# Kernel tuning notes

Measured on AMD Instinct MI355X. Metric: run time of the kernel, lower is better.

The kernel has to match this reference:

```python
import jax, jax.numpy as jnp
import numpy as np

EPS = 1e-8


def normalize_points(p):
    # p: [..., D+1]; normalize feature part to unit L2 norm, fix sign by last coord
    f = p[..., :-1]
    h = p[..., -1:]
    zero_mask = jnp.all(f == 0, axis=-1, keepdims=True)
    f = jnp.where(zero_mask, jnp.ones_like(f), f)
    norm = jnp.linalg.norm(f, axis=-1, keepdims=True)
    nf = f / jnp.clip(norm, EPS)
    n = jnp.concatenate([nf, h], axis=-1)
    sign = jnp.sign(n[..., -1:])
    sign = jnp.where(sign == 0, jnp.ones_like(sign), sign)
    return n * sign


def uhg_transform(x, weight):
    # x: [M, D_in+1], weight: [D_out, D_in]
    f = x[..., :-1]
    h = x[..., -1:]
    t = jnp.matmul(f, weight.T)  # [M, D_out]
    norm = jnp.linalg.norm(t, axis=-1, keepdims=True)
    t = t / jnp.clip(norm, EPS)
    return normalize_points(jnp.concatenate([t, h], axis=-1))


def setup_inputs() -> dict:
    key = jax.random.key(0)
    k1, k2, k3, k4 = jax.random.split(key, 4)
    N, E = 20000, 320000
    D_IN, D_OUT = 256, 256  # in_features-1, out_features
    x = jax.random.normal(k1, (N, D_IN + 1), dtype=jnp.float32)
    edge_index = jax.random.randint(k2, (2, E), 0, N, dtype=jnp.int32)
    # orthogonal-ish init approximated by row-normalized gaussian weights
    W_self = jax.random.normal(k3, (D_OUT, D_IN), dtype=jnp.float32)
    W_self = W_self / jnp.clip(jnp.linalg.norm(W_self, axis=1, keepdims=True), EPS)
    W_neigh = jax.random.normal(k4, (D_OUT, D_IN), dtype=jnp.float32)
    W_neigh = W_neigh / jnp.clip(jnp.linalg.norm(W_neigh, axis=1, keepdims=True), EPS)
    return {"x": x, "W_self": W_self, "W_neigh": W_neigh, "edge_index": edge_index}


def reference(x, W_self, W_neigh, edge_index):
    N = x.shape[0]
    D_OUT = W_self.shape[0]
    x = normalize_points(x)
    row, col = edge_index[0], edge_index[1]

    self_trans = uhg_transform(x, W_self)              # [N, D_OUT+1]
    neigh_trans = uhg_transform(x[col], W_neigh)       # [E, D_OUT+1]

    # mean aggregation: scatter-add full (features + homogeneous), count-divide features only
    out = jnp.zeros((N, D_OUT + 1), dtype=x.dtype).at[:, -1].set(1.0)
    out = out.at[row].add(neigh_trans)
    count = jnp.zeros((N, 1), dtype=x.dtype).at[row].add(1.0)
    count = jnp.clip(count, 1.0)
    out = jnp.concatenate([out[:, :-1] / count, out[:, -1:]], axis=-1)
    out = normalize_points(out)

    # uhg_weighted_average(p1, p2, 0.5): elementwise blend then renormalize
    t = jnp.clip(0.5 / (1.0 - 0.5 + EPS), EPS, 1e8)
    p1 = normalize_points(self_trans)
    p2 = normalize_points(out)
    avg = (p1 * t + p2) / jnp.clip(t + 1.0, EPS)
    combined = normalize_points(avg)
    return normalize_points(combined)
```

## Files before the change

kernel.cpp:

```cpp
#include <hip/hip_runtime.h>
#include <hip/hip_bf16.h>

#define EPSF 1e-8f
#define CAP 64

typedef __attribute__((ext_vector_type(4))) float floatx4;
typedef __attribute__((ext_vector_type(2))) float floatx2;
typedef __attribute__((ext_vector_type(2))) long longx2;

__device__ inline unsigned short f2bf(float v) {
    union { float f; unsigned int u; } un; un.f = v;
    unsigned int r = (un.u + 0x7fffu + ((un.u >> 16) & 1u)) >> 16;
    return (unsigned short)r;
}
__device__ inline float bf2f(unsigned short u) {
    union { unsigned int i; float f; } un; un.i = ((unsigned int)u) << 16;
    return un.f;
}

__device__ inline unsigned char f2fp8(float v) {
#if __has_builtin(__builtin_amdgcn_cvt_pk_fp8_f32)
    return (unsigned char)(__builtin_amdgcn_cvt_pk_fp8_f32(v, 0.f, 0u, false) & 0xff);
#else
    union { float f; unsigned u; } x; x.f = v;
    unsigned s = x.u >> 31; x.u &= 0x7fffffffu;
    if (x.f != x.f || x.f == 0.f) return (unsigned char)(s << 7);
    int e = (int)((x.u >> 23) & 0xff) - 127 + 7;
    unsigned m = x.u & 0x7fffffu;
    unsigned char r;
    if (e >= 1) {
        unsigned keep = m >> 20, rest = m & 0xfffffu;
        keep += (rest > 0x80000u) || (rest == 0x80000u && (keep & 1));
        if (keep == 8) { keep = 0; e += 1; }
        if (e > 15) { e = 15; keep = 6; }
        r = (unsigned char)((e << 3) | keep);
    } else {
        int q = (int)(x.f * 512.f + 0.5f);
        if (q > 7) r = 0x08; else r = (unsigned char)q;
    }
    return (unsigned char)(r | (s << 7));
#endif
}
__device__ inline unsigned pk_fp8x4(float v0, float v1, float v2, float v3) {
#if __has_builtin(__builtin_amdgcn_cvt_pk_fp8_f32)
    unsigned u = __builtin_amdgcn_cvt_pk_fp8_f32(v0, v1, 0u, false);
    u = __builtin_amdgcn_cvt_pk_fp8_f32(v2, v3, u, true);
    return u;
#else
    return (unsigned)f2fp8(v0) | ((unsigned)f2fp8(v1) << 8)
         | ((unsigned)f2fp8(v2) << 16) | ((unsigned)f2fp8(v3) << 24);
#endif
}
__device__ inline floatx2 fp8x2_to_f32(unsigned int u, bool word) {
#if __has_builtin(__builtin_amdgcn_cvt_pk_f32_fp8)
    return word ? __builtin_amdgcn_cvt_pk_f32_fp8(u, true)
                : __builtin_amdgcn_cvt_pk_f32_fp8(u, false);
#else
    floatx2 out;
    #pragma unroll
    for (int i = 0; i < 2; ++i) {
        unsigned char b = (u >> ((word ? 16 : 0) + 8 * i)) & 0xff;
        unsigned s = (b >> 7) & 1, e = (b >> 3) & 15, m = b & 7;
        float v;
        if (e) { union { unsigned u2; float f; } x; x.u2 = (s << 31) | ((e + 120u) << 23) | (m << 20); v = x.f; }
        else   { v = (s ? -1.f : 1.f) * (float)m * 0.001953125f; }
        out[i] = v;
    }
    return out;
#endif
}

__global__ __launch_bounds__(512) void k_front(
        const float* __restrict__ x, const float* __restrict__ Ws,
        const float* __restrict__ Wn,
        unsigned char* __restrict__ Wswz,
        float* __restrict__ xh, int N) {
    int b = blockIdx.x, t = threadIdx.x;
    if (b < 32) {
        int idx = b * 512 + t;
        int t0 = (idx & 3) * 4;
        int lane = (idx >> 2) & 63;
        int p = (idx >> 8) & 3;
        int g = (idx >> 10) & 3;
        int wq = (idx >> 12) & 3;
        int q = lane >> 4, l16 = lane & 15;
        int row = wq * 64 + g * 16 + l16;
        int s = 2 * p + (t0 >> 3);
        int k0 = 32 * s + 8 * q + (t0 & 7);
        float4 vs = *reinterpret_cast<const float4*>(Ws + row * 256 + k0);
        float4 vn = *reinterpret_cast<const float4*>(Wn + row * 256 + k0);
        reinterpret_cast<unsigned*>(Wswz)[idx] = pk_fp8x4(vs.x, vs.y, vs.z, vs.w);
        reinterpret_cast<unsigned*>(Wswz)[16384 + idx] = pk_fp8x4(vn.x, vn.y, vn.z, vn.w);
    } else {
        int i = (b - 32) * 512 + t;
        if (i < N) xh[i] = fabsf(x[(size_t)i * 257 + 256]);
    }
}

__global__ __launch_bounds__(512, 8) void k_mid(
        const float* __restrict__ x,
        const unsigned char* __restrict__ Wswz,
        const int* __restrict__ ei,
        int* __restrict__ cnt, int* __restrict__ scol,
        unsigned short* __restrict__ selfb, unsigned char* __restrict__ yb8,
        int N, int E, int EB) {
    __shared__ __align__(16) unsigned char As[32][256];
    __shared__ float pss[8][32];
    __shared__ float sgnS[32];
    int b = blockIdx.x, tid = threadIdx.x;
    int T = gridDim.x;

    int ebBefore = (int)(((long)b * EB) / T);
    bool isBucket = ((int)(((long)(b + 1) * EB) / T)) != ebBefore;
    if (isBucket) {
        int e = ebBefore * 512 + tid;
        if (e < E) {
            int r = ei[e], c = ei[E + e];
            int pos = atomicAdd(&cnt[r], 1);
            if (pos < CAP) scol[r * CAP + pos] = c;
        }
        return;
    }

    int wave = tid >> 6, lane = tid & 63;
    int quad = lane >> 4, l16 = lane & 15;
    int mat = wave >> 2, wq = wave & 3;
    int row0 = (b - ebBefore) * 32;

    if (tid < 32) {
        int gr = row0 + tid; if (gr >= N) gr = N - 1;
        float h = x[(size_t)gr * 257 + 256];
        sgnS[tid] = (h < 0.f) ? -1.f : 1.f;
    }
    __syncthreads();

    #pragma unroll
    for (int ps = 0; ps < 4; ++ps) {
        int c = ps * 512 + tid;
        int row = c >> 6, k0 = (c & 63) * 4;
        int gr = row0 + row; if (gr >= N) gr = N - 1;
        float4 v = *reinterpret_cast<const float4*>(x + (size_t)gr * 257 + k0);
        float sg = sgnS[row];
        int s = k0 >> 5, q = (k0 >> 3) & 3, j0 = k0 & 7;
        int dst = (q * 64 + (s >> 1) * 16 + (s & 1) * 8 + j0 + row * 16) & 255;
        *reinterpret_cast<unsigned*>(&As[row][dst]) =
            pk_fp8x4(v.x * sg, v.y * sg, v.z * sg, v.w * sg);
    }
    __syncthreads();

    const unsigned char* Wb = Wswz + ((size_t)mat << 16) + ((size_t)wq << 14);
    int rowA = l16, rowB = 16 + l16;

    floatx4 acc[2][4];
    #pragma unroll
    for (int rt = 0; rt < 2; ++rt)
        #pragma unroll
        for (int g = 0; g < 4; ++g) acc[rt][g] = floatx4{0.f, 0.f, 0.f, 0.f};

    #pragma unroll
    for (int p = 0; p < 4; ++p) {
        longx2 a0 = *reinterpret_cast<const longx2*>(
            &As[rowA][(quad * 64 + p * 16 + rowA * 16) & 255]);
        longx2 a1 = *reinterpret_cast<const longx2*>(
            &As[rowB][(quad * 64 + p * 16 + rowB * 16) & 255]);
        #pragma unroll
        for (int g = 0; g < 4; ++g) {
            longx2 w = *reinterpret_cast<const longx2*>(
                Wb + (((g * 4 + p) * 64 + lane) << 4));
            acc[0][g] = __builtin_amdgcn_mfma_f32_16x16x32_fp8_fp8(a0[0], w[0], acc[0][g], 0, 0, 0);
            acc[1][g] = __builtin_amdgcn_mfma_f32_16x16x32_fp8_fp8(a1[0], w[0], acc[1][g], 0, 0, 0);
            acc[0][g] = __builtin_amdgcn_mfma_f32_16x16x32_fp8_fp8(a0[1], w[1], acc[0][g], 0, 0, 0);
            acc[1][g] = __builtin_amdgcn_mfma_f32_16x16x32_fp8_fp8(a1[1], w[1], acc[1][g], 0, 0, 0);
        }
    }

    #pragma unroll
    for (int rt = 0; rt < 2; ++rt) {
        float s[4];
        #pragma unroll
        for (int reg = 0; reg < 4; ++reg) {
            float v = 0.f;
            #pragma unroll
            for (int g = 0; g < 4; ++g) v += acc[rt][g][reg] * acc[rt][g][reg];
            #pragma unroll
            for (int o = 8; o > 0; o >>= 1) v += __shfl_down(v, o, 64);
            s[reg] = v;
        }
        if (l16 == 0) {
            #pragma unroll
            for (int reg = 0; reg < 4; ++reg)
                pss[wave][rt * 16 + quad * 4 + reg] = s[reg];
        }
    }
    __syncthreads();

    int wb = mat * 4;
    #pragma unroll
    for (int rt = 0; rt < 2; ++rt)
        #pragma unroll
        for (int reg = 0; reg < 4; ++reg) {
            int r32 = rt * 16 + quad * 4 + reg;
            int gr = row0 + r32;
            if (gr >= N) continue;
            float ss = pss[wb][r32] + pss[wb + 1][r32]
                     + pss[wb + 2][r32] + pss[wb + 3][r32];
            bool zero = (ss == 0.f);
            float scale = zero ? 0.f : (1.f / fmaxf(sqrtf(ss), EPSF));
            #pragma unroll
            for (int g = 0; g < 4; ++g) {
                int col = wq * 64 + 16 * g + l16;
                float val = zero ? 0.0625f : acc[rt][g][reg] * scale;
                if (mat == 0) selfb[(size_t)gr * 256 + col] = f2bf(val);
                else          yb8[(size_t)gr * 256 + col] = f2fp8(val);
            }
        }
}

__global__ __launch_bounds__(256) void k_agg_combine(
        const int* __restrict__ cnt, const int* __restrict__ scol,
        const unsigned char* __restrict__ yb8,
        const float* __restrict__ xh,
        const unsigned short* __restrict__ selfb,
        float* __restrict__ out, int N) {
    int wid = (blockIdx.x * 256 + threadIdx.x) >> 6;
    if (wid >= N) return;
    int lane = threadIdx.x & 63;
    int deg = cnt[wid]; if (deg > CAP) deg = CAP;
    int beg = wid * CAP;
    float a0 = 0.f, a1 = 0.f, a2 = 0.f, a3 = 0.f;
    float b0 = 0.f, b1 = 0.f, b2 = 0.f, b3 = 0.f;
    int e = beg, end = beg + deg;
    for (; e + 3 < end; e += 4) {
        int c0 = scol[e], c1 = scol[e + 1], c2 = scol[e + 2], c3 = scol[e + 3];
        unsigned u0 = *reinterpret_cast<const unsigned*>(yb8 + (size_t)c0 * 256 + lane * 4);
        unsigned u1 = *reinterpret_cast<const unsigned*>(yb8 + (size_t)c1 * 256 + lane * 4);
        unsigned u2 = *reinterpret_cast<const unsigned*>(yb8 + (size_t)c2 * 256 + lane * 4);
        unsigned u3 = *reinterpret_cast<const unsigned*>(yb8 + (size_t)c3 * 256 + lane * 4);
        floatx2 p;
        p = fp8x2_to_f32(u0, false); a0 += p[0]; a1 += p[1];
        p = fp8x2_to_f32(u0, true);  a2 += p[0]; a3 += p[1];
        p = fp8x2_to_f32(u1, false); b0 += p[0]; b1 += p[1];
        p = fp8x2_to_f32(u1, true);  b2 += p[0]; b3 += p[1];
        p = fp8x2_to_f32(u2, false); a0 += p[0]; a1 += p[1];
        p = fp8x2_to_f32(u2, true);  a2 += p[0]; a3 += p[1];
        p = fp8x2_to_f32(u3, false); b0 += p[0]; b1 += p[1];
        p = fp8x2_to_f32(u3, true);  b2 += p[0]; b3 += p[1];
    }
    for (; e < end; ++e) {
        int c0 = scol[e];
        unsigned u0 = *reinterpret_cast<const unsigned*>(yb8 + (size_t)c0 * 256 + lane * 4);
        floatx2 p;
        p = fp8x2_to_f32(u0, false); a0 += p[0]; a1 += p[1];
        p = fp8x2_to_f32(u0, true);  a2 += p[0]; a3 += p[1];
    }
    a0 += b0; a1 += b1; a2 += b2; a3 += b3;

    float hs = 0.f;
    for (int j = lane; j < deg; j += 64) hs += xh[scol[beg + j]];
    #pragma unroll
    for (int o = 32; o > 0; o >>= 1) hs += __shfl_xor(hs, o, 64);

    float cn = (deg > 0) ? (float)deg : 1.f;
    float m0 = a0 / cn, m1 = a1 / cn, m2 = a2 / cn, m3 = a3 / cn;
    float ss = m0 * m0 + m1 * m1 + m2 * m2 + m3 * m3;
    #pragma unroll
    for (int o = 32; o > 0; o >>= 1) ss += __shfl_xor(ss, o, 64);
    bool z = (ss == 0.f);
    float inv = 1.f / fmaxf(z ? 16.f : sqrtf(ss), EPSF);
    float o0 = (z ? 1.f : m0) * inv, o1 = (z ? 1.f : m1) * inv;
    float o2 = (z ? 1.f : m2) * inv, o3 = (z ? 1.f : m3) * inv;

    ushort4 s4 = *reinterpret_cast<const ushort4*>(selfb + (size_t)wid * 256 + lane * 4);
    float v0 = 0.5f * (bf2f(s4.x) + o0), v1 = 0.5f * (bf2f(s4.y) + o1);
    float v2 = 0.5f * (bf2f(s4.z) + o2), v3 = 0.5f * (bf2f(s4.w) + o3);
    float ss2 = v0 * v0 + v1 * v1 + v2 * v2 + v3 * v3;
    #pragma unroll
    for (int o = 32; o > 0; o >>= 1) ss2 += __shfl_xor(ss2, o, 64);
    bool z2 = (ss2 == 0.f);
    float inv2 = 1.f / fmaxf(z2 ? 16.f : sqrtf(ss2), EPSF);

    float* op = out + (size_t)wid * 257 + lane * 4;
    op[0] = (z2 ? 1.f : v0) * inv2;
    op[1] = (z2 ? 1.f : v1) * inv2;
    op[2] = (z2 ? 1.f : v2) * inv2;
    op[3] = (z2 ? 1.f : v3) * inv2;
    if (lane == 0) out[(size_t)wid * 257 + 256] = 0.5f * (xh[wid] + 1.f + hs);
}

extern "C" void kernel_launch(void* const* d_in, const int* in_sizes, int n_in,
                              void* d_out, int out_size, void* d_ws, size_t ws_size,
                              hipStream_t stream) {
    const float* x  = (const float*)d_in[0];
    const float* Ws = (const float*)d_in[1];
    const float* Wn = (const float*)d_in[2];
    const int*   ei = (const int*)d_in[3];
    int N = in_sizes[0] / 257;
    int E = in_sizes[3] / 2;
    float* out = (float*)d_out;

    char* ws = (char*)d_ws;
    size_t off = 0;
    auto alloc = [&](size_t bytes) {
        void* p = ws + off;
        off = (off + bytes + 255) & ~(size_t)255;
        return p;
    };
    unsigned char* Wswz = (unsigned char*)alloc(131072);
    float* xh    = (float*)alloc((size_t)N * 4);
    unsigned char* yb8 = (unsigned char*)alloc((size_t)N * 256);
    unsigned short* selfb = (unsigned short*)alloc((size_t)N * 256 * 2);
    int* cnt  = (int*)alloc((size_t)N * 4);
    int* scol = (int*)alloc((size_t)N * CAP * 4);

    hipMemsetAsync(cnt, 0, (size_t)N * 4, stream);

    int XB = (N + 511) / 512;
    hipLaunchKernelGGL(k_front, dim3(32 + XB), dim3(512), 0, stream,
                       x, Ws, Wn, Wswz, xh, N);
    int GB = (N + 31) / 32, EB = (E + 511) / 512;
    hipLaunchKernelGGL(k_mid, dim3(GB + EB), dim3(512), 0, stream,
                       x, Wswz, ei, cnt, scol, selfb, yb8, N, E, EB);
    hipLaunchKernelGGL(k_agg_combine, dim3((N + 3) / 4), dim3(256), 0, stream,
                       cnt, scol, yb8, xh, selfb, out, N);
}
```

Baseline: 129.4 us.

## Stage GEMM outputs in LDS for wide stores, widen gather loads, fold memset

The mid kernel now writes its normalized bf16 and fp8 outputs into swizzled shared memory and then stores whole rows with 16-byte vector writes, replacing scattered 1–2 byte global stores. The aggregation kernel switches from 4-byte loads per lane to 16-byte loads, with four lane groups each handling a different neighbour, and combines the partial sums by cross-lane shuffles. The count-array memset is folded into the front kernel, removing one launch. The costs are extra LDS use and a barrier in k_mid, which may reduce occupancy, and more registers plus shuffles in the aggregation. The final output store is done by only a quarter of the lanes.

```diff
diff --git a/kernel.cpp b/kernel.cpp
--- a/kernel.cpp
+++ b/kernel.cpp
@@ -70,11 +70,23 @@
 #endif
 }
 
+__device__ inline void acc16(float* acc, uint4 u) {
+    floatx2 p;
+    p = fp8x2_to_f32(u.x, false); acc[0]  += p[0]; acc[1]  += p[1];
+    p = fp8x2_to_f32(u.x, true);  acc[2]  += p[0]; acc[3]  += p[1];
+    p = fp8x2_to_f32(u.y, false); acc[4]  += p[0]; acc[5]  += p[1];
+    p = fp8x2_to_f32(u.y, true);  acc[6]  += p[0]; acc[7]  += p[1];
+    p = fp8x2_to_f32(u.z, false); acc[8]  += p[0]; acc[9]  += p[1];
+    p = fp8x2_to_f32(u.z, true);  acc[10] += p[0]; acc[11] += p[1];
+    p = fp8x2_to_f32(u.w, false); acc[12] += p[0]; acc[13] += p[1];
+    p = fp8x2_to_f32(u.w, true);  acc[14] += p[0]; acc[15] += p[1];
+}
+
 __global__ __launch_bounds__(512) void k_front(
         const float* __restrict__ x, const float* __restrict__ Ws,
         const float* __restrict__ Wn,
         unsigned char* __restrict__ Wswz,
-        float* __restrict__ xh, int N) {
+        float* __restrict__ xh, int* __restrict__ cnt, int N) {
     int b = blockIdx.x, t = threadIdx.x;
     if (b < 32) {
         int idx = b * 512 + t;
@@ -93,7 +105,10 @@
         reinterpret_cast<unsigned*>(Wswz)[16384 + idx] = pk_fp8x4(vn.x, vn.y, vn.z, vn.w);
     } else {
         int i = (b - 32) * 512 + t;
-        if (i < N) xh[i] = fabsf(x[(size_t)i * 257 + 256]);
+        if (i < N) {
+            xh[i] = fabsf(x[(size_t)i * 257 + 256]);
+            cnt[i] = 0;
+        }
     }
 }
 
@@ -105,6 +120,7 @@
         unsigned short* __restrict__ selfb, unsigned char* __restrict__ yb8,
         int N, int E, int EB) {
     __shared__ __align__(16) unsigned char As[32][256];
+    __shared__ __align__(16) unsigned short sOut[32][256];
     __shared__ float pss[8][32];
     __shared__ float sgnS[32];
     int b = blockIdx.x, tid = threadIdx.x;
@@ -200,20 +216,37 @@
         #pragma unroll
         for (int reg = 0; reg < 4; ++reg) {
             int r32 = rt * 16 + quad * 4 + reg;
-            int gr = row0 + r32;
-            if (gr >= N) continue;
             float ss = pss[wb][r32] + pss[wb + 1][r32]
                      + pss[wb + 2][r32] + pss[wb + 3][r32];
             bool zero = (ss == 0.f);
             float scale = zero ? 0.f : (1.f / fmaxf(sqrtf(ss), EPSF));
+            int xb = ((r32 >> 2) & 3) << 4;
             #pragma unroll
             for (int g = 0; g < 4; ++g) {
                 int col = wq * 64 + 16 * g + l16;
                 float val = zero ? 0.0625f : acc[rt][g][reg] * scale;
-                if (mat == 0) selfb[(size_t)gr * 256 + col] = f2bf(val);
-                else          yb8[(size_t)gr * 256 + col] = f2fp8(val);
+                int cs = col ^ xb;
+                if (mat == 0) sOut[r32][cs] = f2bf(val);
+                else          As[r32][cs]   = f2fp8(val);
             }
         }
+    __syncthreads();
+
+    {
+        int r = tid >> 4;
+        int gr = row0 + r;
+        if (gr < N) {
+            int blk = (tid & 15) ^ ((r >> 2) & 3);
+            int cb  = blk * 16;
+            int cbo = (tid & 15) * 16;
+            uint4 a0 = *reinterpret_cast<const uint4*>(&sOut[r][cb]);
+            uint4 a1 = *reinterpret_cast<const uint4*>(&sOut[r][cb + 8]);
+            *reinterpret_cast<uint4*>(selfb + (size_t)gr * 256 + cbo) = a0;
+            *reinterpret_cast<uint4*>(selfb + (size_t)gr * 256 + cbo + 8) = a1;
+            uint4 y0 = *reinterpret_cast<const uint4*>(&As[r][cb]);
+            *reinterpret_cast<uint4*>(yb8 + (size_t)gr * 256 + cbo) = y0;
+        }
+    }
 }
 
 __global__ __launch_bounds__(256) void k_agg_combine(
@@ -225,35 +258,42 @@
     int wid = (blockIdx.x * 256 + threadIdx.x) >> 6;
     if (wid >= N) return;
     int lane = threadIdx.x & 63;
+    int g = lane >> 4, l16 = lane & 15;
     int deg = cnt[wid]; if (deg > CAP) deg = CAP;
     int beg = wid * CAP;
-    float a0 = 0.f, a1 = 0.f, a2 = 0.f, a3 = 0.f;
-    float b0 = 0.f, b1 = 0.f, b2 = 0.f, b3 = 0.f;
-    int e = beg, end = beg + deg;
-    for (; e + 3 < end; e += 4) {
-        int c0 = scol[e], c1 = scol[e + 1], c2 = scol[e + 2], c3 = scol[e + 3];
-        unsigned u0 = *reinterpret_cast<const unsigned*>(yb8 + (size_t)c0 * 256 + lane * 4);
-        unsigned u1 = *reinterpret_cast<const unsigned*>(yb8 + (size_t)c1 * 256 + lane * 4);
-        unsigned u2 = *reinterpret_cast<const unsigned*>(yb8 + (size_t)c2 * 256 + lane * 4);
-        unsigned u3 = *reinterpret_cast<const unsigned*>(yb8 + (size_t)c3 * 256 + lane * 4);
-        floatx2 p;
-        p = fp8x2_to_f32(u0, false); a0 += p[0]; a1 += p[1];
-        p = fp8x2_to_f32(u0, true);  a2 += p[0]; a3 += p[1];
-        p = fp8x2_to_f32(u1, false); b0 += p[0]; b1 += p[1];
-        p = fp8x2_to_f32(u1, true);  b2 += p[0]; b3 += p[1];
-        p = fp8x2_to_f32(u2, false); a0 += p[0]; a1 += p[1];
-        p = fp8x2_to_f32(u2, true);  a2 += p[0]; a3 += p[1];
-        p = fp8x2_to_f32(u3, false); b0 += p[0]; b1 += p[1];
-        p = fp8x2_to_f32(u3, true);  b2 += p[0]; b3 += p[1];
-    }
-    for (; e < end; ++e) {
-        int c0 = scol[e];
-        unsigned u0 = *reinterpret_cast<const unsigned*>(yb8 + (size_t)c0 * 256 + lane * 4);
-        floatx2 p;
-        p = fp8x2_to_f32(u0, false); a0 += p[0]; a1 += p[1];
-        p = fp8x2_to_f32(u0, true);  a2 += p[0]; a3 += p[1];
-    }
-    a0 += b0; a1 += b1; a2 += b2; a3 += b3;
+
+    float acc[16];
+    #pragma unroll
+    for (int j = 0; j < 16; ++j) acc[j] = 0.f;
+
+    int e = 0;
+    for (; e + 8 <= deg; e += 8) {
+        int c0 = scol[beg + e + g];
+        int c1 = scol[beg + e + 4 + g];
+        uint4 u0 = *reinterpret_cast<const uint4*>(yb8 + (size_t)c0 * 256 + l16 * 16);
+        uint4 u1 = *reinterpret_cast<const uint4*>(yb8 + (size_t)c1 * 256 + l16 * 16);
+        acc16(acc, u0);
+        acc16(acc, u1);
+    }
+    if (e < deg) {
+        int i0 = e + g;
+        if (i0 < deg) {
+            int c = scol[beg + i0];
+            uint4 u = *reinterpret_cast<const uint4*>(yb8 + (size_t)c * 256 + l16 * 16);
+            acc16(acc, u);
+        }
+        int i1 = e + 4 + g;
+        if (i1 < deg) {
+            int c = scol[beg + i1];
+            uint4 u = *reinterpret_cast<const uint4*>(yb8 + (size_t)c * 256 + l16 * 16);
+            acc16(acc, u);
+        }
+    }
+    #pragma unroll
+    for (int j = 0; j < 16; ++j) {
+        acc[j] += __shfl_xor(acc[j], 16, 64);
+        acc[j] += __shfl_xor(acc[j], 32, 64);
+    }
 
     float hs = 0.f;
     for (int j = lane; j < deg; j += 64) hs += xh[scol[beg + j]];
@@ -261,29 +301,42 @@
     for (int o = 32; o > 0; o >>= 1) hs += __shfl_xor(hs, o, 64);
 
     float cn = (deg > 0) ? (float)deg : 1.f;
-    float m0 = a0 / cn, m1 = a1 / cn, m2 = a2 / cn, m3 = a3 / cn;
-    float ss = m0 * m0 + m1 * m1 + m2 * m2 + m3 * m3;
-    #pragma unroll
-    for (int o = 32; o > 0; o >>= 1) ss += __shfl_xor(ss, o, 64);
+    float rcn = 1.f / cn;
+    float m_[16];
+    float ss = 0.f;
+    #pragma unroll
+    for (int j = 0; j < 16; ++j) { m_[j] = acc[j] * rcn; ss += m_[j] * m_[j]; }
+    #pragma unroll
+    for (int o = 1; o < 16; o <<= 1) ss += __shfl_xor(ss, o, 64);
     bool z = (ss == 0.f);
     float inv = 1.f / fmaxf(z ? 16.f : sqrtf(ss), EPSF);
-    float o0 = (z ? 1.f : m0) * inv, o1 = (z ? 1.f : m1) * inv;
-    float o2 = (z ? 1.f : m2) * inv, o3 = (z ? 1.f : m3) * inv;
-
-    ushort4 s4 = *reinterpret_cast<const ushort4*>(selfb + (size_t)wid * 256 + lane * 4);
-    float v0 = 0.5f * (bf2f(s4.x) + o0), v1 = 0.5f * (bf2f(s4.y) + o1);
-    float v2 = 0.5f * (bf2f(s4.z) + o2), v3 = 0.5f * (bf2f(s4.w) + o3);
-    float ss2 = v0 * v0 + v1 * v1 + v2 * v2 + v3 * v3;
-    #pragma unroll
-    for (int o = 32; o > 0; o >>= 1) ss2 += __shfl_xor(ss2, o, 64);
+
+    const unsigned short* sp = selfb + (size_t)wid * 256 + l16 * 16;
+    uint4 s0 = *reinterpret_cast<const uint4*>(sp);
+    uint4 s1 = *reinterpret_cast<const uint4*>(sp + 8);
+    unsigned sw[8] = { s0.x, s0.y, s0.z, s0.w, s1.x, s1.y, s1.z, s1.w };
+    float v_[16];
+    float ss2 = 0.f;
+    #pragma unroll
+    for (int j = 0; j < 8; ++j) {
+        float slo = bf2f((unsigned short)(sw[j] & 0xffff));
+        float shi = bf2f((unsigned short)(sw[j] >> 16));
+        float olo = (z ? 1.f : m_[2 * j]) * inv;
+        float ohi = (z ? 1.f : m_[2 * j + 1]) * inv;
+        v_[2 * j]     = 0.5f * (slo + olo);
+        v_[2 * j + 1] = 0.5f * (shi + ohi);
+        ss2 += v_[2 * j] * v_[2 * j] + v_[2 * j + 1] * v_[2 * j + 1];
+    }
+    #pragma unroll
+    for (int o = 1; o < 16; o <<= 1) ss2 += __shfl_xor(ss2, o, 64);
     bool z2 = (ss2 == 0.f);
     float inv2 = 1.f / fmaxf(z2 ? 16.f : sqrtf(ss2), EPSF);
 
-    float* op = out + (size_t)wid * 257 + lane * 4;
-    op[0] = (z2 ? 1.f : v0) * inv2;
-    op[1] = (z2 ? 1.f : v1) * inv2;
-    op[2] = (z2 ? 1.f : v2) * inv2;
-    op[3] = (z2 ? 1.f : v3) * inv2;
+    if (g == 0) {
+        float* op = out + (size_t)wid * 257 + l16 * 16;
+        #pragma unroll
+        for (int j = 0; j < 16; ++j) op[j] = (z2 ? 1.f : v_[j]) * inv2;
+    }
     if (lane == 0) out[(size_t)wid * 257 + 256] = 0.5f * (xh[wid] + 1.f + hs);
 }
 
@@ -312,11 +365,9 @@
     int* cnt  = (int*)alloc((size_t)N * 4);
     int* scol = (int*)alloc((size_t)N * CAP * 4);
 
-    hipMemsetAsync(cnt, 0, (size_t)N * 4, stream);
-
     int XB = (N + 511) / 512;
     hipLaunchKernelGGL(k_front, dim3(32 + XB), dim3(512), 0, stream,
-                       x, Ws, Wn, Wswz, xh, N);
+                       x, Ws, Wn, Wswz, xh, cnt, N);
     int GB = (N + 31) / 32, EB = (E + 511) / 512;
     hipLaunchKernelGGL(k_mid, dim3(GB + EB), dim3(512), 0, stream,
                        x, Wswz, ei, cnt, scol, selfb, yb8, N, E, EB);
```

Result: faster. 125.6 us (-2.9%).
